# Optimization experiments

Measured on AMD Instinct MI355X. Metric: run time of the kernel, lower is better.

## Reference

```python
import jax, jax.numpy as jnp
import numpy as np

WS = 8            # window size (square)
NUM_HEADS = 8
DIM = 256
IMG = 256         # feature map H=W for mask construction
SHIFT = WS // 2
B = 4


def _rel_pos_index(Wh, Ww):
    coords = np.stack(np.meshgrid(np.arange(Wh), np.arange(Ww), indexing='ij'))  # (2,Wh,Ww)
    cf = coords.reshape(2, -1)
    rel = cf[:, :, None] - cf[:, None, :]        # (2,N,N)
    rel = rel.transpose(1, 2, 0).astype(np.int64)
    rel[..., 0] += Wh - 1
    rel[..., 1] += Ww - 1
    rel[..., 0] *= 2 * Ww - 1
    return rel.sum(-1)                           # (N,N)


def _shift_mask(H, W, ws, ss):
    # standard Swin shifted-window attention mask: (nW, ws*ws, ws*ws) with 0 / -100
    img = np.zeros((H, W), dtype=np.float32)
    cnt = 0
    for hs in (slice(0, -ws), slice(-ws, -ss), slice(-ss, None)):
        for wsl in (slice(0, -ws), slice(-ws, -ss), slice(-ss, None)):
            img[hs, wsl] = cnt
            cnt += 1
    m = img.reshape(H // ws, ws, W // ws, ws).transpose(0, 2, 1, 3).reshape(-1, ws * ws)
    am = m[:, None, :] - m[:, :, None]
    return np.where(am != 0, np.float32(-100.0), np.float32(0.0))


def setup_inputs() -> dict:
    key = jax.random.key(0)
    ks = jax.random.split(key, 10)
    nW = (IMG // WS) ** 2
    B_ = B * nW
    N = WS * WS
    x = jax.random.normal(ks[0], (B_, N, DIM), dtype=jnp.float32)
    y = jax.random.normal(ks[1], (B_, N, DIM), dtype=jnp.float32)
    mask = jnp.asarray(_shift_mask(IMG, IMG, WS, SHIFT))
    s = 0.02
    q_w = jax.random.normal(ks[2], (DIM, DIM), dtype=jnp.float32) * s
    q_b = jnp.zeros((DIM,), dtype=jnp.float32)
    kv_w = jax.random.normal(ks[3], (2 * DIM, DIM), dtype=jnp.float32) * s
    kv_b = jnp.zeros((2 * DIM,), dtype=jnp.float32)
    proj_w = jax.random.normal(ks[4], (DIM, DIM), dtype=jnp.float32) * s
    proj_b = jnp.zeros((DIM,), dtype=jnp.float32)
    rpb_table = jax.random.normal(ks[5], ((2 * WS - 1) ** 2, NUM_HEADS), dtype=jnp.float32) * s
    return {"x": x, "y": y, "mask": mask, "q_w": q_w, "q_b": q_b,
            "kv_w": kv_w, "kv_b": kv_b, "proj_w": proj_w, "proj_b": proj_b,
            "rpb_table": rpb_table}


def reference(x, y, mask, q_w, q_b, kv_w, kv_b, proj_w, proj_b, rpb_table):
    B_, N, C = x.shape
    H = NUM_HEADS
    hd = C // H
    scale = hd ** -0.5
    # projections
    q = (x @ q_w.T + q_b).reshape(B_, N, H, hd).transpose(0, 2, 1, 3) * scale  # (B_,H,N,hd)
    kv = (y @ kv_w.T + kv_b).reshape(B_, N, 2, H, hd)
    k = kv[:, :, 0].transpose(0, 2, 1, 3)  # (B_,H,N,hd)
    v = kv[:, :, 1].transpose(0, 2, 1, 3)
    attn = jnp.einsum('bhid,bhjd->bhij', q, k)  # (B_,H,N,N)
    # relative position bias gathered from table
    rpi = jnp.asarray(_rel_pos_index(WS, WS))           # (N,N) int
    bias = rpb_table[rpi.reshape(-1)].reshape(N, N, H).transpose(2, 0, 1)  # (H,N,N)
    attn = attn + bias[None]
    # shifted-window mask
    nW = mask.shape[0]
    attn = attn.reshape(B_ // nW, nW, H, N, N) + mask[None, :, None]
    attn = attn.reshape(B_, H, N, N)
    attn = jax.nn.softmax(attn, axis=-1)
    out = jnp.einsum('bhij,bhjd->bhid', attn, v)        # (B_,H,N,hd)
    out = out.transpose(0, 2, 1, 3).reshape(B_, N, C)
    return out @ proj_w.T + proj_b
```

## Files before the change

### kernel.cpp

```cpp
#include <hip/hip_runtime.h>

typedef _Float16 half_t;
typedef _Float16 half8  __attribute__((ext_vector_type(8)));
typedef _Float16 half4v __attribute__((ext_vector_type(4)));
typedef float    f32x4  __attribute__((ext_vector_type(4)));

#define ROWB   528
#define S_A    0
#define S_B    33792
#define SMEM_BYTES 67584
#define SCALE  0.17677669529663687f

__global__ __launch_bounds__(256) void swin_prep(
    const float* __restrict__ q_w, const float* __restrict__ kv_w,
    const float* __restrict__ proj_w, const float* __restrict__ rpb,
    const float* __restrict__ mask,
    half_t* __restrict__ w16, half_t* __restrict__ fused)
{
    int t = blockIdx.x * 256 + threadIdx.x;
    if (t < 65536)        w16[t] = (half_t)(q_w[t] * SCALE);
    else if (t < 196608)  w16[t] = (half_t)kv_w[t - 65536];
    else if (t < 262144)  w16[t] = (half_t)proj_w[t - 196608];
    else if (t < 393216) {
        int u = t - 262144;
        int cls = u >> 15, rest = u & 32767;
        int h = rest >> 12, i = (rest >> 6) & 63, j = rest & 63;
        int idx = ((i >> 3) - (j >> 3) + 7) * 15 + ((i & 7) - (j & 7) + 7);
        int wsel = (cls == 0) ? 0 : (cls == 1) ? 31 : (cls == 2) ? 992 : 1023;
        fused[u] = (half_t)(rpb[idx * 8 + h] + mask[(size_t)wsel * 4096 + i * 64 + j]);
    }
}

static __device__ __forceinline__ unsigned pk2(float a, float b) {
    union { _Float16 h[2]; unsigned u; } t;
    t.h[0] = (_Float16)a; t.h[1] = (_Float16)b; return t.u;
}

#define BUILD_FRAG(dst, P0, P1)                                          \
    do {                                                                 \
        union { unsigned u[4]; half8 h; } _u;                            \
        _Pragma("unroll")                                                \
        for (int p = 0; p < 4; ++p) {                                    \
            int _src = (p >> 1) ? srcB : srcA;                           \
            unsigned _rlo = (unsigned)__shfl((int)(P0)[p & 1], _src);    \
            unsigned _rhi = (unsigned)__shfl((int)(P1)[p & 1], _src);    \
            _u.u[p] = hi ? _rhi : _rlo;                                  \
        }                                                                \
        dst = _u.h;                                                      \
    } while (0)

__global__ __launch_bounds__(512, 4) void swin_main(
    const float* __restrict__ x, const float* __restrict__ y,
    const float* __restrict__ q_b, const float* __restrict__ kv_b,
    const float* __restrict__ proj_b,
    const half_t* __restrict__ w16, const half_t* __restrict__ fused,
    float* __restrict__ out)
{
    __shared__ __align__(16) char sm[SMEM_BYTES];
    const int tid  = threadIdx.x;
    const int w    = tid >> 6;
    const int lane = tid & 63;
    const int l15  = lane & 15;
    const int g    = lane >> 4;
    const int b    = blockIdx.x;
    const int jf0  = w * 32;
    const int srcA = ((2 * g) & 3) * 16 + l15;
    const int srcB = ((2 * g + 1) & 3) * 16 + l15;
    const int hi   = g >> 1;

    const float* xb = x + (size_t)b * 16384;
    const float* yb = y + (size_t)b * 16384;
    const half_t* wkv = w16 + 65536;

    {
        float4 fx[8], fy[8];
        #pragma unroll
        for (int it = 0; it < 4; ++it) {
            int c = tid + it * 512;
            int row = c >> 5, c8 = c & 31;
            fx[it*2+0] = *(const float4*)(xb + row * 256 + c8 * 8);
            fx[it*2+1] = *(const float4*)(xb + row * 256 + c8 * 8 + 4);
            fy[it*2+0] = *(const float4*)(yb + row * 256 + c8 * 8);
            fy[it*2+1] = *(const float4*)(yb + row * 256 + c8 * 8 + 4);
        }
        #pragma unroll
        for (int it = 0; it < 4; ++it) {
            int c = tid + it * 512;
            int row = c >> 5, c8 = c & 31;
            half8 hx, hy;
            #pragma unroll
            for (int e = 0; e < 4; ++e) {
                hx[e]   = (half_t)(&fx[it*2+0].x)[e];
                hx[e+4] = (half_t)(&fx[it*2+1].x)[e];
                hy[e]   = (half_t)(&fy[it*2+0].x)[e];
                hy[e+4] = (half_t)(&fy[it*2+1].x)[e];
            }
            int off = row * ROWB + c8 * 16;
            *(half8*)(sm + S_A + off) = hx;
            *(half8*)(sm + S_B + off) = hy;
        }
    }
    __syncthreads();

    f32x4 kacc[2][4], vacc[4][2];
    #pragma unroll
    for (int ft = 0; ft < 2; ++ft)
        #pragma unroll
        for (int tok = 0; tok < 4; ++tok) {
            f32x4 z = {0.f,0.f,0.f,0.f}; kacc[ft][tok] = z; vacc[tok][ft] = z;
        }
    #pragma unroll
    for (int kh = 0; kh < 2; ++kh) {
        half8 wbk[4][2], wbv[4][2];
        #pragma unroll
        for (int k2 = 0; k2 < 4; ++k2) {
            int k0 = (kh * 4 + k2) * 32 + g * 8;
            #pragma unroll
            for (int ft = 0; ft < 2; ++ft) {
                int jf = jf0 + ft * 16 + l15;
                wbk[k2][ft] = *(const half8*)(wkv + jf * 256 + k0);
                wbv[k2][ft] = *(const half8*)(wkv + (256 + jf) * 256 + k0);
            }
        }
        #pragma unroll
        for (int k2 = 0; k2 < 4; ++k2) {
            int k0 = (kh * 4 + k2) * 32 + g * 8;
            half8 a[4];
            #pragma unroll
            for (int tok = 0; tok < 4; ++tok)
                a[tok] = *(const half8*)(sm + S_B + (tok * 16 + l15) * ROWB + k0 * 2);
            #pragma unroll
            for (int ft = 0; ft < 2; ++ft)
                #pragma unroll
                for (int tok = 0; tok < 4; ++tok) {
                    kacc[ft][tok] = __builtin_amdgcn_mfma_f32_16x16x32_f16(wbk[k2][ft], a[tok], kacc[ft][tok], 0, 0, 0);
                    vacc[tok][ft] = __builtin_amdgcn_mfma_f32_16x16x32_f16(a[tok], wbv[k2][ft], vacc[tok][ft], 0, 0, 0);
                }
        }
    }
    __syncthreads();

    unsigned kp[2][4][2], vp[4][2][2];
    {
        #pragma unroll
        for (int ft = 0; ft < 2; ++ft) {
            float4 kb4 = *(const float4*)(kv_b + jf0 + ft * 16 + g * 4);
            #pragma unroll
            for (int tok = 0; tok < 4; ++tok) {
                kp[ft][tok][0] = pk2(kacc[ft][tok][0] + kb4.x, kacc[ft][tok][1] + kb4.y);
                kp[ft][tok][1] = pk2(kacc[ft][tok][2] + kb4.z, kacc[ft][tok][3] + kb4.w);
            }
        }
        #pragma unroll
        for (int ft = 0; ft < 2; ++ft) {
            float vb = kv_b[256 + jf0 + ft * 16 + l15];
            #pragma unroll
            for (int tok = 0; tok < 4; ++tok) {
                vp[tok][ft][0] = pk2(vacc[tok][ft][0] + vb, vacc[tok][ft][1] + vb);
                vp[tok][ft][1] = pk2(vacc[tok][ft][2] + vb, vacc[tok][ft][3] + vb);
            }
        }
    }

    unsigned qp[2][4][2];
    {
        f32x4 qacc[2][4];
        #pragma unroll
        for (int ft = 0; ft < 2; ++ft)
            #pragma unroll
            for (int tok = 0; tok < 4; ++tok) { f32x4 z = {0.f,0.f,0.f,0.f}; qacc[ft][tok] = z; }
        #pragma unroll
        for (int kh = 0; kh < 2; ++kh) {
            half8 wbq[4][2];
            #pragma unroll
            for (int k2 = 0; k2 < 4; ++k2) {
                int k0 = (kh * 4 + k2) * 32 + g * 8;
                #pragma unroll
                for (int ft = 0; ft < 2; ++ft)
                    wbq[k2][ft] = *(const half8*)(w16 + (jf0 + ft * 16 + l15) * 256 + k0);
            }
            #pragma unroll
            for (int k2 = 0; k2 < 4; ++k2) {
                int k0 = (kh * 4 + k2) * 32 + g * 8;
                half8 a[4];
                #pragma unroll
                for (int tok = 0; tok < 4; ++tok)
                    a[tok] = *(const half8*)(sm + S_A + (tok * 16 + l15) * ROWB + k0 * 2);
                #pragma unroll
                for (int ft = 0; ft < 2; ++ft)
                    #pragma unroll
                    for (int tok = 0; tok < 4; ++tok)
                        qacc[ft][tok] = __builtin_amdgcn_mfma_f32_16x16x32_f16(wbq[k2][ft], a[tok], qacc[ft][tok], 0, 0, 0);
            }
        }
        #pragma unroll
        for (int ft = 0; ft < 2; ++ft) {
            float4 qb4 = *(const float4*)(q_b + jf0 + ft * 16 + g * 4);
            #pragma unroll
            for (int tok = 0; tok < 4; ++tok) {
                qp[ft][tok][0] = pk2(qacc[ft][tok][0] + qb4.x * SCALE, qacc[ft][tok][1] + qb4.y * SCALE);
                qp[ft][tok][1] = pk2(qacc[ft][tok][2] + qb4.z * SCALE, qacc[ft][tok][3] + qb4.w * SCALE);
            }
        }
    }

    {
        const int wi = b & 1023;
        const int cls = ((((wi >> 5) == 31) ? 2 : 0)) | (((wi & 31) == 31) ? 1 : 0);
        const half_t* fb = fused + ((size_t)cls * 8 + w) * 4096;

        half4v fm[4][4];
        #pragma unroll
        for (int nt = 0; nt < 4; ++nt)
            #pragma unroll
            for (int mt = 0; mt < 4; ++mt)
                fm[nt][mt] = *(const half4v*)(fb + (nt * 16 + l15) * 64 + mt * 16 + g * 4);

        half8 ka[4], qf[4];
        #pragma unroll
        for (int mt = 0; mt < 4; ++mt) BUILD_FRAG(ka[mt], kp[0][mt], kp[1][mt]);
        #pragma unroll
        for (int nt = 0; nt < 4; ++nt) BUILD_FRAG(qf[nt], qp[0][nt], qp[1][nt]);

        f32x4 t[4][4];
        #pragma unroll
        for (int mt = 0; mt < 4; ++mt)
            #pragma unroll
            for (int nt = 0; nt < 4; ++nt) {
                f32x4 z = {0.f,0.f,0.f,0.f};
                t[mt][nt] = __builtin_amdgcn_mfma_f32_16x16x32_f16(ka[mt], qf[nt], z, 0, 0, 0);
            }

        #pragma unroll
        for (int nt = 0; nt < 4; ++nt) {
            #pragma unroll
            for (int mt = 0; mt < 4; ++mt)
                #pragma unroll
                for (int r = 0; r < 4; ++r)
                    t[mt][nt][r] += (float)fm[nt][mt][r];
            float m = -1e30f;
            #pragma unroll
            for (int mt = 0; mt < 4; ++mt)
                #pragma unroll
                for (int r = 0; r < 4; ++r) m = fmaxf(m, t[mt][nt][r]);
            m = fmaxf(m, __shfl_xor(m, 16));
            m = fmaxf(m, __shfl_xor(m, 32));
            float s = 0.f;
            #pragma unroll
            for (int mt = 0; mt < 4; ++mt)
                #pragma unroll
                for (int r = 0; r < 4; ++r) {
                    float p = __expf(t[mt][nt][r] - m);
                    t[mt][nt][r] = p;
                    s += p;
                }
            s += __shfl_xor(s, 16);
            s += __shfl_xor(s, 32);
            float inv = 1.f / s;
            #pragma unroll
            for (int mt = 0; mt < 4; ++mt)
                #pragma unroll
                for (int r = 0; r < 4; ++r) t[mt][nt][r] *= inv;
        }

        unsigned pp[4][4][2];
        #pragma unroll
        for (int mt = 0; mt < 4; ++mt)
            #pragma unroll
            for (int nt = 0; nt < 4; ++nt) {
                pp[mt][nt][0] = pk2(t[mt][nt][0], t[mt][nt][1]);
                pp[mt][nt][1] = pk2(t[mt][nt][2], t[mt][nt][3]);
            }

        f32x4 o[2][4];
        #pragma unroll
        for (int dt = 0; dt < 2; ++dt)
            #pragma unroll
            for (int nt = 0; nt < 4; ++nt) { f32x4 z = {0.f,0.f,0.f,0.f}; o[dt][nt] = z; }
        #pragma unroll
        for (int kc = 0; kc < 2; ++kc) {
            half8 va[2], pf[4];
            #pragma unroll
            for (int dt = 0; dt < 2; ++dt) BUILD_FRAG(va[dt], vp[kc*2+0][dt], vp[kc*2+1][dt]);
            #pragma unroll
            for (int nt = 0; nt < 4; ++nt) BUILD_FRAG(pf[nt], pp[kc*2+0][nt], pp[kc*2+1][nt]);
            #pragma unroll
            for (int dt = 0; dt < 2; ++dt)
                #pragma unroll
                for (int nt = 0; nt < 4; ++nt)
                    o[dt][nt] = __builtin_amdgcn_mfma_f32_16x16x32_f16(va[dt], pf[nt], o[dt][nt], 0, 0, 0);
        }

        half8 wbp[8][2];
        #pragma unroll
        for (int kc = 0; kc < 8; ++kc) {
            int k0 = kc * 32 + g * 8;
            #pragma unroll
            for (int ft = 0; ft < 2; ++ft)
                wbp[kc][ft] = *(const half8*)(w16 + 196608 + (jf0 + ft * 16 + l15) * 256 + k0);
        }

        #pragma unroll
        for (int nt = 0; nt < 4; ++nt) {
            int i = nt * 16 + l15;
            #pragma unroll
            for (int dt = 0; dt < 2; ++dt) {
                half4v ov;
                ov[0] = (half_t)o[dt][nt][0];
                ov[1] = (half_t)o[dt][nt][1];
                ov[2] = (half_t)o[dt][nt][2];
                ov[3] = (half_t)o[dt][nt][3];
                *(half4v*)(sm + S_B + i * ROWB + (jf0 + dt * 16 + g * 4) * 2) = ov;
            }
        }
        __syncthreads();

        f32x4 acc[4][2];
        #pragma unroll
        for (int mt = 0; mt < 4; ++mt)
            #pragma unroll
            for (int ft = 0; ft < 2; ++ft) { f32x4 z = {0.f,0.f,0.f,0.f}; acc[mt][ft] = z; }
        #pragma unroll
        for (int kc = 0; kc < 8; ++kc) {
            int k0 = kc * 32 + g * 8;
            half8 a[4];
            #pragma unroll
            for (int mt = 0; mt < 4; ++mt)
                a[mt] = *(const half8*)(sm + S_B + (mt * 16 + l15) * ROWB + k0 * 2);
            #pragma unroll
            for (int mt = 0; mt < 4; ++mt)
                #pragma unroll
                for (int ft = 0; ft < 2; ++ft)
                    acc[mt][ft] = __builtin_amdgcn_mfma_f32_16x16x32_f16(a[mt], wbp[kc][ft], acc[mt][ft], 0, 0, 0);
        }
        float* ob = out + (size_t)b * 16384;
        #pragma unroll
        for (int ft = 0; ft < 2; ++ft) {
            int jf = jf0 + ft * 16 + l15;
            float pbv = proj_b[jf];
            #pragma unroll
            for (int mt = 0; mt < 4; ++mt)
                #pragma unroll
                for (int r = 0; r < 4; ++r) {
                    int i = mt * 16 + g * 4 + r;
                    ob[i * 256 + jf] = acc[mt][ft][r] + pbv;
                }
        }
    }
}

extern "C" void kernel_launch(void* const* d_in, const int* in_sizes, int n_in,
                              void* d_out, int out_size, void* d_ws, size_t ws_size,
                              hipStream_t stream) {
    const float* x      = (const float*)d_in[0];
    const float* y      = (const float*)d_in[1];
    const float* mask   = (const float*)d_in[2];
    const float* q_w    = (const float*)d_in[3];
    const float* q_b    = (const float*)d_in[4];
    const float* kv_w   = (const float*)d_in[5];
    const float* kv_b   = (const float*)d_in[6];
    const float* proj_w = (const float*)d_in[7];
    const float* proj_b = (const float*)d_in[8];
    const float* rpb    = (const float*)d_in[9];

    half_t* w16   = (half_t*)d_ws;
    half_t* fused = (half_t*)((char*)d_ws + 524288);

    swin_prep<<<1536, 256, 0, stream>>>(q_w, kv_w, proj_w, rpb, mask, w16, fused);
    swin_main<<<4096, 512, 0, stream>>>(x, y, q_b, kv_b, proj_b,
                                        w16, fused, (float*)d_out);
}
```

Baseline: 518.1 us.

## Cut register pressure, reorder attention loads, vectorize output stores in swin kernel

Lowers the launch-bounds occupancy hint from 4 to 2 blocks per CU and splits weight prefetch into smaller chunks (2 k-steps instead of 4), which reduces live weight registers. It drops the sync after the KV projection, issues the QK MFMAs before loading the fused bias/mask, and moves the proj-weight loads into the projection loop. The output projection now swaps MFMA operands so each lane writes float4 rows of output, giving coalesced vector stores in place of scalar ones. The smaller weight prefetch may expose more global-load latency, and the lower occupancy hint may allow fewer concurrent waves.

```diff
diff --git a/kernel.cpp b/kernel.cpp
--- a/kernel.cpp
+++ b/kernel.cpp
@@ -49,7 +49,7 @@
         dst = _u.h;                                                      \
     } while (0)
 
-__global__ __launch_bounds__(512, 4) void swin_main(
+__global__ __launch_bounds__(512, 2) void swin_main(
     const float* __restrict__ x, const float* __restrict__ y,
     const float* __restrict__ q_b, const float* __restrict__ kv_b,
     const float* __restrict__ proj_b,
@@ -110,11 +110,11 @@
             f32x4 z = {0.f,0.f,0.f,0.f}; kacc[ft][tok] = z; vacc[tok][ft] = z;
         }
     #pragma unroll
-    for (int kh = 0; kh < 2; ++kh) {
-        half8 wbk[4][2], wbv[4][2];
-        #pragma unroll
-        for (int k2 = 0; k2 < 4; ++k2) {
-            int k0 = (kh * 4 + k2) * 32 + g * 8;
+    for (int kh = 0; kh < 4; ++kh) {
+        half8 wbk[2][2], wbv[2][2];
+        #pragma unroll
+        for (int k2 = 0; k2 < 2; ++k2) {
+            int k0 = (kh * 2 + k2) * 32 + g * 8;
             #pragma unroll
             for (int ft = 0; ft < 2; ++ft) {
                 int jf = jf0 + ft * 16 + l15;
@@ -123,8 +123,8 @@
             }
         }
         #pragma unroll
-        for (int k2 = 0; k2 < 4; ++k2) {
-            int k0 = (kh * 4 + k2) * 32 + g * 8;
+        for (int k2 = 0; k2 < 2; ++k2) {
+            int k0 = (kh * 2 + k2) * 32 + g * 8;
             half8 a[4];
             #pragma unroll
             for (int tok = 0; tok < 4; ++tok)
@@ -138,27 +138,24 @@
                 }
         }
     }
-    __syncthreads();
 
     unsigned kp[2][4][2], vp[4][2][2];
-    {
-        #pragma unroll
-        for (int ft = 0; ft < 2; ++ft) {
-            float4 kb4 = *(const float4*)(kv_b + jf0 + ft * 16 + g * 4);
-            #pragma unroll
-            for (int tok = 0; tok < 4; ++tok) {
-                kp[ft][tok][0] = pk2(kacc[ft][tok][0] + kb4.x, kacc[ft][tok][1] + kb4.y);
-                kp[ft][tok][1] = pk2(kacc[ft][tok][2] + kb4.z, kacc[ft][tok][3] + kb4.w);
-            }
-        }
-        #pragma unroll
-        for (int ft = 0; ft < 2; ++ft) {
-            float vb = kv_b[256 + jf0 + ft * 16 + l15];
-            #pragma unroll
-            for (int tok = 0; tok < 4; ++tok) {
-                vp[tok][ft][0] = pk2(vacc[tok][ft][0] + vb, vacc[tok][ft][1] + vb);
-                vp[tok][ft][1] = pk2(vacc[tok][ft][2] + vb, vacc[tok][ft][3] + vb);
-            }
+    #pragma unroll
+    for (int ft = 0; ft < 2; ++ft) {
+        float4 kb4 = *(const float4*)(kv_b + jf0 + ft * 16 + g * 4);
+        #pragma unroll
+        for (int tok = 0; tok < 4; ++tok) {
+            kp[ft][tok][0] = pk2(kacc[ft][tok][0] + kb4.x, kacc[ft][tok][1] + kb4.y);
+            kp[ft][tok][1] = pk2(kacc[ft][tok][2] + kb4.z, kacc[ft][tok][3] + kb4.w);
+        }
+    }
+    #pragma unroll
+    for (int ft = 0; ft < 2; ++ft) {
+        float vb = kv_b[256 + jf0 + ft * 16 + l15];
+        #pragma unroll
+        for (int tok = 0; tok < 4; ++tok) {
+            vp[tok][ft][0] = pk2(vacc[tok][ft][0] + vb, vacc[tok][ft][1] + vb);
+            vp[tok][ft][1] = pk2(vacc[tok][ft][2] + vb, vacc[tok][ft][3] + vb);
         }
     }
 
@@ -170,18 +167,18 @@
             #pragma unroll
             for (int tok = 0; tok < 4; ++tok) { f32x4 z = {0.f,0.f,0.f,0.f}; qacc[ft][tok] = z; }
         #pragma unroll
-        for (int kh = 0; kh < 2; ++kh) {
-            half8 wbq[4][2];
-            #pragma unroll
-            for (int k2 = 0; k2 < 4; ++k2) {
-                int k0 = (kh * 4 + k2) * 32 + g * 8;
+        for (int kh = 0; kh < 4; ++kh) {
+            half8 wbq[2][2];
+            #pragma unroll
+            for (int k2 = 0; k2 < 2; ++k2) {
+                int k0 = (kh * 2 + k2) * 32 + g * 8;
                 #pragma unroll
                 for (int ft = 0; ft < 2; ++ft)
                     wbq[k2][ft] = *(const half8*)(w16 + (jf0 + ft * 16 + l15) * 256 + k0);
             }
             #pragma unroll
-            for (int k2 = 0; k2 < 4; ++k2) {
-                int k0 = (kh * 4 + k2) * 32 + g * 8;
+            for (int k2 = 0; k2 < 2; ++k2) {
+                int k0 = (kh * 2 + k2) * 32 + g * 8;
                 half8 a[4];
                 #pragma unroll
                 for (int tok = 0; tok < 4; ++tok)
@@ -204,32 +201,32 @@
         }
     }
 
+    f32x4 o[2][4];
     {
+        half8 ka[4], qf[4];
+        #pragma unroll
+        for (int mt = 0; mt < 4; ++mt) BUILD_FRAG(ka[mt], kp[0][mt], kp[1][mt]);
+        #pragma unroll
+        for (int nt = 0; nt < 4; ++nt) BUILD_FRAG(qf[nt], qp[0][nt], qp[1][nt]);
+
+        f32x4 t[4][4];
+        #pragma unroll
+        for (int mt = 0; mt < 4; ++mt)
+            #pragma unroll
+            for (int nt = 0; nt < 4; ++nt) {
+                f32x4 z = {0.f,0.f,0.f,0.f};
+                t[mt][nt] = __builtin_amdgcn_mfma_f32_16x16x32_f16(ka[mt], qf[nt], z, 0, 0, 0);
+            }
+
         const int wi = b & 1023;
         const int cls = ((((wi >> 5) == 31) ? 2 : 0)) | (((wi & 31) == 31) ? 1 : 0);
         const half_t* fb = fused + ((size_t)cls * 8 + w) * 4096;
-
         half4v fm[4][4];
         #pragma unroll
         for (int nt = 0; nt < 4; ++nt)
             #pragma unroll
             for (int mt = 0; mt < 4; ++mt)
                 fm[nt][mt] = *(const half4v*)(fb + (nt * 16 + l15) * 64 + mt * 16 + g * 4);
-
-        half8 ka[4], qf[4];
-        #pragma unroll
-        for (int mt = 0; mt < 4; ++mt) BUILD_FRAG(ka[mt], kp[0][mt], kp[1][mt]);
-        #pragma unroll
-        for (int nt = 0; nt < 4; ++nt) BUILD_FRAG(qf[nt], qp[0][nt], qp[1][nt]);
-
-        f32x4 t[4][4];
-        #pragma unroll
-        for (int mt = 0; mt < 4; ++mt)
-            #pragma unroll
-            for (int nt = 0; nt < 4; ++nt) {
-                f32x4 z = {0.f,0.f,0.f,0.f};
-                t[mt][nt] = __builtin_amdgcn_mfma_f32_16x16x32_f16(ka[mt], qf[nt], z, 0, 0, 0);
-            }
 
         #pragma unroll
         for (int nt = 0; nt < 4; ++nt) {
@@ -272,7 +269,6 @@
                 pp[mt][nt][1] = pk2(t[mt][nt][2], t[mt][nt][3]);
             }
 
-        f32x4 o[2][4];
         #pragma unroll
         for (int dt = 0; dt < 2; ++dt)
             #pragma unroll
@@ -290,61 +286,69 @@
                 for (int nt = 0; nt < 4; ++nt)
                     o[dt][nt] = __builtin_amdgcn_mfma_f32_16x16x32_f16(va[dt], pf[nt], o[dt][nt], 0, 0, 0);
         }
-
-        half8 wbp[8][2];
-        #pragma unroll
-        for (int kc = 0; kc < 8; ++kc) {
-            int k0 = kc * 32 + g * 8;
-            #pragma unroll
-            for (int ft = 0; ft < 2; ++ft)
-                wbp[kc][ft] = *(const half8*)(w16 + 196608 + (jf0 + ft * 16 + l15) * 256 + k0);
-        }
-
-        #pragma unroll
-        for (int nt = 0; nt < 4; ++nt) {
-            int i = nt * 16 + l15;
-            #pragma unroll
-            for (int dt = 0; dt < 2; ++dt) {
-                half4v ov;
-                ov[0] = (half_t)o[dt][nt][0];
-                ov[1] = (half_t)o[dt][nt][1];
-                ov[2] = (half_t)o[dt][nt][2];
-                ov[3] = (half_t)o[dt][nt][3];
-                *(half4v*)(sm + S_B + i * ROWB + (jf0 + dt * 16 + g * 4) * 2) = ov;
-            }
-        }
-        __syncthreads();
-
-        f32x4 acc[4][2];
+    }
+
+    __syncthreads();
+
+    #pragma unroll
+    for (int nt = 0; nt < 4; ++nt) {
+        int i = nt * 16 + l15;
+        #pragma unroll
+        for (int dt = 0; dt < 2; ++dt) {
+            half4v ov;
+            ov[0] = (half_t)o[dt][nt][0];
+            ov[1] = (half_t)o[dt][nt][1];
+            ov[2] = (half_t)o[dt][nt][2];
+            ov[3] = (half_t)o[dt][nt][3];
+            *(half4v*)(sm + S_B + i * ROWB + (jf0 + dt * 16 + g * 4) * 2) = ov;
+        }
+    }
+    __syncthreads();
+
+    {
+        const half_t* wp = w16 + 196608;
+        f32x4 dacc[4][2];
         #pragma unroll
         for (int mt = 0; mt < 4; ++mt)
             #pragma unroll
-            for (int ft = 0; ft < 2; ++ft) { f32x4 z = {0.f,0.f,0.f,0.f}; acc[mt][ft] = z; }
-        #pragma unroll
-        for (int kc = 0; kc < 8; ++kc) {
-            int k0 = kc * 32 + g * 8;
-            half8 a[4];
-            #pragma unroll
-            for (int mt = 0; mt < 4; ++mt)
-                a[mt] = *(const half8*)(sm + S_B + (mt * 16 + l15) * ROWB + k0 * 2);
-            #pragma unroll
-            for (int mt = 0; mt < 4; ++mt)
+            for (int ft = 0; ft < 2; ++ft) { f32x4 z = {0.f,0.f,0.f,0.f}; dacc[mt][ft] = z; }
+        #pragma unroll
+        for (int kh = 0; kh < 4; ++kh) {
+            half8 wbp[2][2];
+            #pragma unroll
+            for (int k2 = 0; k2 < 2; ++k2) {
+                int k0 = (kh * 2 + k2) * 32 + g * 8;
                 #pragma unroll
                 for (int ft = 0; ft < 2; ++ft)
-                    acc[mt][ft] = __builtin_amdgcn_mfma_f32_16x16x32_f16(a[mt], wbp[kc][ft], acc[mt][ft], 0, 0, 0);
+                    wbp[k2][ft] = *(const half8*)(wp + (jf0 + ft * 16 + l15) * 256 + k0);
+            }
+            #pragma unroll
+            for (int k2 = 0; k2 < 2; ++k2) {
+                int k0 = (kh * 2 + k2) * 32 + g * 8;
+                half8 a[4];
+                #pragma unroll
+                for (int mt = 0; mt < 4; ++mt)
+                    a[mt] = *(const half8*)(sm + S_B + (mt * 16 + l15) * ROWB + k0 * 2);
+                #pragma unroll
+                for (int mt = 0; mt < 4; ++mt)
+                    #pragma unroll
+                    for (int ft = 0; ft < 2; ++ft)
+                        dacc[mt][ft] = __builtin_amdgcn_mfma_f32_16x16x32_f16(wbp[k2][ft], a[mt], dacc[mt][ft], 0, 0, 0);
+            }
         }
         float* ob = out + (size_t)b * 16384;
         #pragma unroll
         for (int ft = 0; ft < 2; ++ft) {
-            int jf = jf0 + ft * 16 + l15;
-            float pbv = proj_b[jf];
-            #pragma unroll
-            for (int mt = 0; mt < 4; ++mt)
-                #pragma unroll
-                for (int r = 0; r < 4; ++r) {
-                    int i = mt * 16 + g * 4 + r;
-                    ob[i * 256 + jf] = acc[mt][ft][r] + pbv;
-                }
+            float4 pb4 = *(const float4*)(proj_b + jf0 + ft * 16 + g * 4);
+            #pragma unroll
+            for (int mt = 0; mt < 4; ++mt) {
+                float4 v;
+                v.x = dacc[mt][ft][0] + pb4.x;
+                v.y = dacc[mt][ft][1] + pb4.y;
+                v.z = dacc[mt][ft][2] + pb4.z;
+                v.w = dacc[mt][ft][3] + pb4.w;
+                *(float4*)(ob + (mt * 16 + l15) * 256 + jf0 + ft * 16 + g * 4) = v;
+            }
         }
     }
 }
```

Result: faster. 469.4 us (-9.4%).
